# Kernel optimization log

Hardware: AMD Instinct MI355X
Metric: run time of the kernel (lower is better)

## Reference

```python
import jax, jax.numpy as jnp
import numpy as np

SIGMA_DIS = 3.0
MAX_LABELS = 33  # label ids in [0, 32]; 0 = background, 1..32 = kernels


def setup_inputs() -> dict:
    key = jax.random.key(0)
    k1, k2 = jax.random.split(key)
    B, C, H, W = 8, 4, 896, 896
    pred = jax.random.normal(k1, (B, C, H, W), dtype=jnp.float32)
    kernels_mask = jnp.ones((B, H, W), dtype=jnp.float32)
    labels = jax.random.randint(k2, (B, H, W), 0, MAX_LABELS, dtype=jnp.int32)
    return {
        "pred_similarities": pred,
        "kernels_mask": kernels_mask,
        "kernel_mask_ndi_labels": labels,
    }


def _disc_loss(pred, labels, sigma):
    # pred: [B, C, H, W], labels: [B, H, W] int
    B, C = pred.shape[0], pred.shape[1]
    p = pred.reshape(B, C, -1)        # [B, C, N]
    lab = labels.reshape(B, -1)       # [B, N]

    # Masks for distinct labels are disjoint, so for a = pred*mask_i/|K_i|,
    # b = pred*mask_j/|K_j|:  ||a - b||_F^2 = s_i + s_j where
    # s_k = sum_{pixels in K_k} sum_c pred^2 / |K_k|^2.
    sq = jnp.sum(p * p, axis=1)       # [B, N]

    def seg(x, l):
        return jax.ops.segment_sum(x, l, num_segments=MAX_LABELS)

    card = jax.vmap(seg)(jnp.ones_like(sq), lab)   # [B, L] pixel counts
    ssq = jax.vmap(seg)(sq, lab)                   # [B, L] sum of squares
    safe_card = jnp.where(card > 0, card, 1.0)
    s = ssq / (safe_card * safe_card)              # [B, L]

    nk = jnp.max(lab, axis=1)                      # [B] num_kernels per image
    ks = jnp.arange(MAX_LABELS)
    valid = (ks[None, :] >= 1) & (ks[None, :] <= nk[:, None]) & (card > 0)  # [B, L]

    # all unordered pairs i < j of valid labels
    pair_mask = (
        valid[:, :, None] & valid[:, None, :] & (ks[:, None] < ks[None, :])[None]
    )  # [B, L, L]
    S = s[:, :, None] + s[:, None, :]
    S_safe = jnp.where(pair_mask, S, 1.0)          # keep sqrt grads finite
    # NOTE: original torch.max(norm, 0)[0] on a 0-d tensor is a dim-reduction
    # over a size-1 view and is an identity, NOT a clamp; replicated faithfully.
    d = sigma - jnp.sqrt(S_safe)
    term = jnp.log(d * d + 1.0)
    per_b = jnp.sum(jnp.where(pair_mask, term, 0.0), axis=(1, 2))  # [B]

    nk_f = nk.astype(per_b.dtype)
    denom = jnp.where(nk > 1, nk_f * (nk_f - 1.0), 1.0)
    loss_b = jnp.where(nk > 1, per_b / denom, 0.0)
    return jnp.sum(loss_b)


def reference(pred_similarities, kernels_mask, kernel_mask_ndi_labels):
    # kernels_mask is reshaped but never used by the original forward math.
    return _disc_loss(pred_similarities, kernel_mask_ndi_labels, SIGMA_DIS)
```

## Files before the change

### kernel.cpp

```cpp
#include <hip/hip_runtime.h>

#define MAXL 33
#define CSTR 36
#define PB 128
#define TPB 128

__global__ __launch_bounds__(TPB, 3) void seg_hist_kernel(
    const float* __restrict__ pred, const int* __restrict__ labels,
    float* __restrict__ partial, int N) {
  const int b = blockIdx.y;
  const int ng = N >> 2;
  __shared__ float sumh[TPB * MAXL];
  __shared__ unsigned char cnth[TPB * CSTR];
  __shared__ float xred[2][2][MAXL];
  const int tid = threadIdx.x;

  float* sh = &sumh[tid * MAXL];
  unsigned char* ch = &cnth[tid * CSTR];
#pragma unroll
  for (int i = 0; i < MAXL; ++i) sh[i] = 0.f;
#pragma unroll
  for (int i = 0; i < CSTR / 4; ++i)
    reinterpret_cast<unsigned*>(ch)[i] = 0u;

  const float4* p = reinterpret_cast<const float4*>(pred) + (size_t)b * 4 * ng;
  const int4* lb = reinterpret_cast<const int4*>(labels) + (size_t)b * ng;
  const int STRIDE = PB * TPB;

  int g = blockIdx.x * TPB + tid;
  float4 c0 = p[g], c1 = p[g + ng], c2 = p[g + 2 * ng], c3 = p[g + 3 * ng];
  int4 l = lb[g];

  while (true) {
    const int gn = g + STRIDE;
    const bool more = gn < ng;
    float4 n0, n1, n2, n3;
    int4 nl;
    if (more) {
      n0 = p[gn];
      n1 = p[gn + ng];
      n2 = p[gn + 2 * ng];
      n3 = p[gn + 3 * ng];
      nl = lb[gn];
    }

    float s0 = c0.x * c0.x + c1.x * c1.x + c2.x * c2.x + c3.x * c3.x;
    float s1 = c0.y * c0.y + c1.y * c1.y + c2.y * c2.y + c3.y * c3.y;
    float s2 = c0.z * c0.z + c1.z * c1.z + c2.z * c2.z + c3.z * c3.z;
    float s3 = c0.w * c0.w + c1.w * c1.w + c2.w * c2.w + c3.w * c3.w;

    const bool e01 = l.x == l.y, e02 = l.x == l.z, e03 = l.x == l.w;
    const bool e12 = l.y == l.z, e13 = l.y == l.w, e23 = l.z == l.w;
    const float w1 = s1 + (e01 ? s0 : 0.f);
    const float w2 = s2 + (e12 ? s1 : 0.f) + (e02 ? s0 : 0.f);
    const float w3 =
        s3 + (e23 ? s2 : 0.f) + (e13 ? s1 : 0.f) + (e03 ? s0 : 0.f);
    const unsigned m1 = 1u + (unsigned)e01;
    const unsigned m2 = 1u + (unsigned)e12 + (unsigned)e02;
    const unsigned m3 = 1u + (unsigned)e23 + (unsigned)e13 + (unsigned)e03;

    const float r0 = sh[l.x], r1 = sh[l.y], r2 = sh[l.z], r3 = sh[l.w];
    const unsigned q0 = ch[l.x], q1 = ch[l.y], q2 = ch[l.z], q3 = ch[l.w];
    sh[l.x] = r0 + s0;
    sh[l.y] = r1 + w1;
    sh[l.z] = r2 + w2;
    sh[l.w] = r3 + w3;
    ch[l.x] = (unsigned char)(q0 + 1u);
    ch[l.y] = (unsigned char)(q1 + m1);
    ch[l.z] = (unsigned char)(q2 + m2);
    ch[l.w] = (unsigned char)(q3 + m3);

    if (!more) break;
    c0 = n0;
    c1 = n1;
    c2 = n2;
    c3 = n3;
    l = nl;
    g = gn;
  }
  __syncthreads();

  const int wave = tid >> 6;
  const int lane = tid & 63;
  if (lane < MAXL) {
    float fs = 0.f;
    unsigned fc = 0u;
#pragma unroll 8
    for (int u = 0; u < 64; ++u) {
      fs += sumh[(wave * 64 + u) * MAXL + lane];
      fc += (unsigned)cnth[(wave * 64 + u) * CSTR + lane];
    }
    xred[wave][0][lane] = fs;
    xred[wave][1][lane] = (float)fc;
  }
  __syncthreads();
  if (tid < MAXL) {
    partial[(size_t)(b * 2 * MAXL + tid) * PB + blockIdx.x] =
        xred[0][0][tid] + xred[1][0][tid];
    partial[(size_t)(b * 2 * MAXL + MAXL + tid) * PB + blockIdx.x] =
        xred[0][1][tid] + xred[1][1][tid];
  }
}

__global__ __launch_bounds__(512) void reduce_finalize_kernel(
    const float* __restrict__ partial, float* __restrict__ out) {
  __shared__ float red[8 * 2 * MAXL];
  __shared__ float s_val[8 * MAXL];
  __shared__ float s_flag[8 * MAXL];
  __shared__ float s_invden[8];
  __shared__ float s_part[8];
  const int tid = threadIdx.x;
  const int wave = tid >> 6;
  const int lane = tid & 63;

  {
    int slot = tid;
    const float4* row =
        reinterpret_cast<const float4*>(partial) + (size_t)slot * (PB / 4);
    float a0 = 0.f, a1 = 0.f;
#pragma unroll 8
    for (int u = 0; u < PB / 4; u += 2) {
      float4 x = row[u], y = row[u + 1];
      a0 += x.x + x.y + x.z + x.w;
      a1 += y.x + y.y + y.z + y.w;
    }
    if (slot < 8 * 2 * MAXL) red[slot] = a0 + a1;
  }
  if (tid < 8 * 2 * MAXL - 512) {
    int slot = 512 + tid;
    const float4* row =
        reinterpret_cast<const float4*>(partial) + (size_t)slot * (PB / 4);
    float a0 = 0.f, a1 = 0.f;
#pragma unroll 8
    for (int u = 0; u < PB / 4; u += 2) {
      float4 x = row[u], y = row[u + 1];
      a0 += x.x + x.y + x.z + x.w;
      a1 += y.x + y.y + y.z + y.w;
    }
    red[slot] = a0 + a1;
  }
  __syncthreads();

  for (int i = tid; i < 8 * MAXL; i += 512) {
    int b = i / MAXL, l = i - b * MAXL;
    float cnt = red[b * 2 * MAXL + MAXL + l];
    float ssq = red[b * 2 * MAXL + l];
    float safe = cnt > 0.f ? cnt : 1.f;
    s_val[i] = ssq / (safe * safe);
    s_flag[i] = (l >= 1 && cnt > 0.f) ? 1.f : 0.f;
  }
  __syncthreads();
  if (tid < 8) {
    int nk = 0;
    for (int l = MAXL - 1; l >= 0; --l) {
      if (red[tid * 2 * MAXL + MAXL + l] > 0.f) {
        nk = l;
        break;
      }
    }
    s_invden[tid] = (nk > 1) ? 1.f / ((float)nk * ((float)nk - 1.f)) : 0.f;
  }
  __syncthreads();

  float local = 0.f;
  const int total = 8 * MAXL * MAXL;
  for (int idx = tid; idx < total; idx += 512) {
    int b = idx / (MAXL * MAXL);
    int r = idx - b * MAXL * MAXL;
    int i = r / MAXL;
    int j = r - i * MAXL;
    if (i < j && s_flag[b * MAXL + i] != 0.f && s_flag[b * MAXL + j] != 0.f) {
      float S = s_val[b * MAXL + i] + s_val[b * MAXL + j];
      float d = 3.0f - sqrtf(S);
      local += logf(d * d + 1.f) * s_invden[b];
    }
  }
  for (int off = 32; off; off >>= 1) local += __shfl_down(local, off, 64);
  if (lane == 0) s_part[wave] = local;
  __syncthreads();
  if (tid == 0) {
    float tot = 0.f;
    for (int w = 0; w < 8; ++w) tot += s_part[w];
    out[0] = tot;
  }
}

extern "C" void kernel_launch(void* const* d_in, const int* in_sizes, int n_in,
                              void* d_out, int out_size, void* d_ws,
                              size_t ws_size, hipStream_t stream) {
  const float* pred = (const float*)d_in[0];
  const int* labels = (const int*)d_in[2];
  float* out = (float*)d_out;

  const int B = 8;
  const int N = in_sizes[2] / B;

  float* partial = (float*)d_ws;

  dim3 grid(PB, B);
  seg_hist_kernel<<<grid, dim3(TPB), 0, stream>>>(pred, labels, partial, N);
  reduce_finalize_kernel<<<dim3(1), dim3(512), 0, stream>>>(partial, out);
}
```

Baseline: 40.00 us.

## Fully unroll histogram loop with triple-buffered loads for fixed image size

Replaces the generic strided while-loop with a fixed 12-13 iteration unrolled schedule that keeps three iterations of loads in flight (A/B/C register buffers). This targets memory latency by raising memory-level parallelism per thread. The occupancy hint drops from 3 to 2 blocks per CU to allow the extra registers. The schedule hardcodes the trip count for N=896*896 (ng/GSTR about 12.25), so other input sizes would be processed incorrectly.

Result: no change. 39.58 us (-1.1%).

```diff
diff --git a/kernel.cpp b/kernel.cpp
--- a/kernel.cpp
+++ b/kernel.cpp
@@ -4,8 +4,9 @@
 #define CSTR 36
 #define PB 128
 #define TPB 128
-
-__global__ __launch_bounds__(TPB, 3) void seg_hist_kernel(
+#define GSTR (PB * TPB)
+
+__global__ __launch_bounds__(TPB, 2) void seg_hist_kernel(
     const float* __restrict__ pred, const int* __restrict__ labels,
     float* __restrict__ partial, int N) {
   const int b = blockIdx.y;
@@ -20,35 +21,27 @@
 #pragma unroll
   for (int i = 0; i < MAXL; ++i) sh[i] = 0.f;
 #pragma unroll
-  for (int i = 0; i < CSTR / 4; ++i)
-    reinterpret_cast<unsigned*>(ch)[i] = 0u;
+  for (int i = 0; i < CSTR / 4; ++i) reinterpret_cast<unsigned*>(ch)[i] = 0u;
 
   const float4* p = reinterpret_cast<const float4*>(pred) + (size_t)b * 4 * ng;
   const int4* lb = reinterpret_cast<const int4*>(labels) + (size_t)b * ng;
-  const int STRIDE = PB * TPB;
-
-  int g = blockIdx.x * TPB + tid;
-  float4 c0 = p[g], c1 = p[g + ng], c2 = p[g + 2 * ng], c3 = p[g + 3 * ng];
-  int4 l = lb[g];
-
-  while (true) {
-    const int gn = g + STRIDE;
-    const bool more = gn < ng;
-    float4 n0, n1, n2, n3;
-    int4 nl;
-    if (more) {
-      n0 = p[gn];
-      n1 = p[gn + ng];
-      n2 = p[gn + 2 * ng];
-      n3 = p[gn + 3 * ng];
-      nl = lb[gn];
-    }
-
+  const int start = blockIdx.x * TPB + tid;
+  const bool has13 = (start + 12 * GSTR) < ng;
+
+  auto ld = [&](int g, float4& c0, float4& c1, float4& c2, float4& c3,
+                int4& l) {
+    c0 = p[g];
+    c1 = p[g + ng];
+    c2 = p[g + 2 * ng];
+    c3 = p[g + 3 * ng];
+    l = lb[g];
+  };
+  auto proc = [&](const float4& c0, const float4& c1, const float4& c2,
+                  const float4& c3, const int4& l) {
     float s0 = c0.x * c0.x + c1.x * c1.x + c2.x * c2.x + c3.x * c3.x;
     float s1 = c0.y * c0.y + c1.y * c1.y + c2.y * c2.y + c3.y * c3.y;
     float s2 = c0.z * c0.z + c1.z * c1.z + c2.z * c2.z + c3.z * c3.z;
     float s3 = c0.w * c0.w + c1.w * c1.w + c2.w * c2.w + c3.w * c3.w;
-
     const bool e01 = l.x == l.y, e02 = l.x == l.z, e03 = l.x == l.w;
     const bool e12 = l.y == l.z, e13 = l.y == l.w, e23 = l.z == l.w;
     const float w1 = s1 + (e01 ? s0 : 0.f);
@@ -58,7 +51,6 @@
     const unsigned m1 = 1u + (unsigned)e01;
     const unsigned m2 = 1u + (unsigned)e12 + (unsigned)e02;
     const unsigned m3 = 1u + (unsigned)e23 + (unsigned)e13 + (unsigned)e03;
-
     const float r0 = sh[l.x], r1 = sh[l.y], r2 = sh[l.z], r3 = sh[l.w];
     const unsigned q0 = ch[l.x], q1 = ch[l.y], q2 = ch[l.z], q3 = ch[l.w];
     sh[l.x] = r0 + s0;
@@ -69,15 +61,29 @@
     ch[l.y] = (unsigned char)(q1 + m1);
     ch[l.z] = (unsigned char)(q2 + m2);
     ch[l.w] = (unsigned char)(q3 + m3);
-
-    if (!more) break;
-    c0 = n0;
-    c1 = n1;
-    c2 = n2;
-    c3 = n3;
-    l = nl;
-    g = gn;
-  }
+  };
+
+  float4 A0, A1, A2, A3, B0, B1, B2, B3, C0, C1, C2, C3;
+  int4 Al, Bl, Cl;
+
+  ld(start + 0 * GSTR, A0, A1, A2, A3, Al);
+  ld(start + 1 * GSTR, B0, B1, B2, B3, Bl);
+  ld(start + 2 * GSTR, C0, C1, C2, C3, Cl);
+
+#pragma unroll
+  for (int k = 0; k < 3; ++k) {
+    proc(A0, A1, A2, A3, Al);
+    ld(start + (3 * k + 3) * GSTR, A0, A1, A2, A3, Al);
+    proc(B0, B1, B2, B3, Bl);
+    ld(start + (3 * k + 4) * GSTR, B0, B1, B2, B3, Bl);
+    proc(C0, C1, C2, C3, Cl);
+    ld(start + (3 * k + 5) * GSTR, C0, C1, C2, C3, Cl);
+  }
+  proc(A0, A1, A2, A3, Al);
+  if (has13) ld(start + 12 * GSTR, A0, A1, A2, A3, Al);
+  proc(B0, B1, B2, B3, Bl);
+  proc(C0, C1, C2, C3, Cl);
+  if (has13) proc(A0, A1, A2, A3, Al);
   __syncthreads();
 
   const int wave = tid >> 6;
```
